# Kernel optimization log

Hardware: AMD Instinct MI355X
Metric: run time of the kernel (lower is better)

## Reference

```python
import jax, jax.numpy as jnp
import numpy as np

EPS = 1e-6
HEADS = 8


def _block_weights(gh, gw):
    # block centers at (i+0.5, j+0.5); 'cos' transform, column-normalized (sum over dim 0)
    ii, jj = np.meshgrid(np.arange(gh) + 0.5, np.arange(gw) + 0.5, indexing='ij')
    centers = np.stack([ii.ravel(), jj.ravel()], axis=-1)  # [N, 2]
    d = np.linalg.norm(centers[:, None, :] - centers[None, :, :], axis=-1)  # [N, N]
    mat = np.cos(d / d.max() * np.pi / 4.0)
    mat = mat / mat.sum(axis=0, keepdims=True)
    return jnp.asarray(mat, dtype=jnp.float32)


def setup_inputs() -> dict:
    key = jax.random.key(0)
    ks = jax.random.split(key, 5)
    B, N, W, C = 8, 256, 49, 512
    s = 1.0 / np.sqrt(C)
    return {
        'x': jax.random.normal(ks[0], (B, N, W, C), jnp.float32),
        'ln_g': jnp.ones((C,), jnp.float32),
        'ln_b': jnp.zeros((C,), jnp.float32),
        'w_qkv': jax.random.normal(ks[1], (3 * C, C), jnp.float32) * s,  # Linear(dim, 3*dim, bias=False)
        'lepe_w': jax.random.normal(ks[2], (C, 1, 5, 5), jnp.float32) * 0.2,  # depthwise 5x5
        'lepe_b': jnp.zeros((C,), jnp.float32),
        'w_out': jax.random.normal(ks[3], (C, C), jnp.float32) * s,
        'b_out': jnp.zeros((C,), jnp.float32),
    }


def reference(x, ln_g, ln_b, w_qkv, lepe_w, lepe_b, w_out, b_out):
    B, N, Wn, C = x.shape
    H = HEADS
    D = C // H
    gh = gw = int(round(N ** 0.5))   # grid of window blocks
    wh = ww = int(round(Wn ** 0.5))  # tokens per window side

    # LayerNorm over channel dim (torch eps=1e-5, biased var)
    mu = x.mean(-1, keepdims=True)
    var = x.var(-1, keepdims=True)
    xn = (x - mu) / jnp.sqrt(var + 1e-5) * ln_g + ln_b

    # qkv projection
    qkv = jnp.einsum('bnwc,oc->bnwo', xn, w_qkv)
    q, k, v = jnp.split(qkv, 3, axis=-1)  # each [B, N, W, C]

    # LePE: fold v to image [B, C, gh*wh, gw*ww], depthwise conv 5x5 pad 2, unfold back
    img = v.reshape(B, gh, gw, wh, ww, C).transpose(0, 5, 1, 3, 2, 4).reshape(B, C, gh * wh, gw * ww)
    lepe = jax.lax.conv_general_dilated(
        img, lepe_w, window_strides=(1, 1), padding=((2, 2), (2, 2)),
        dimension_numbers=('NCHW', 'OIHW', 'NCHW'), feature_group_count=C)
    lepe = lepe + lepe_b[None, :, None, None]
    lepe = lepe.reshape(B, C, gh, wh, gw, ww).transpose(0, 2, 4, 3, 5, 1).reshape(B, N, Wn, C)

    # ReLU + eps feature maps (qk_norm=False -> identity norms)
    q = jax.nn.relu(q) + EPS
    k = jax.nn.relu(k) + EPS

    # split heads: [B, H, N, W, D]
    def split_heads(t):
        return t.reshape(B, N, Wn, H, D).transpose(0, 3, 1, 2, 4)
    q, k, v = split_heads(q), split_heads(k), split_heads(v)

    # per-block k^T v state: [B, H, N, D, D]
    kv = jnp.einsum('bhnwd,bhnwe->bhnde', k, v)
    weight = _block_weights(gh, gw)  # [N, N]
    kv = jnp.einsum('ij,bhjde->bhide', weight, kv)

    k_sum = k.sum(axis=-2)  # [B, H, N, D]
    qk_sum = jnp.einsum('bhnwd,bhnd->bhnw', q, k_sum)[..., None]  # [B, H, N, W, 1]
    normalizer = jnp.einsum('ij,bhjwo->bhiwo', weight, qk_sum) + EPS

    out = jnp.einsum('bhnwd,bhnde->bhnwe', q, kv) / normalizer  # [B, H, N, W, D]
    out = out.transpose(0, 2, 3, 1, 4).reshape(B, N, Wn, C)
    out = out + lepe
    return jnp.einsum('bnwc,oc->bnwo', out, w_out) + b_out
```

## Files before the change

kernel.cpp:

```cpp
#include <hip/hip_runtime.h>
#include <cstdint>

typedef unsigned short u16;
typedef unsigned int   u32;
typedef u16   u16x8 __attribute__((ext_vector_type(8)));
typedef u16   u16x4 __attribute__((ext_vector_type(4)));
typedef float f32x4 __attribute__((ext_vector_type(4)));
typedef __bf16 bf16x8 __attribute__((ext_vector_type(8)));

#define NB    256
#define WTOK  49
#define CH    512
#define HEADS 8
#define DH    64
#define TOK   100352

__device__ __forceinline__ u16 f2bf(float f) {
  u32 u = __float_as_uint(f);
  u = (u + 0x7FFFu + ((u >> 16) & 1u)) >> 16;
  return (u16)u;
}
__device__ __forceinline__ float bf2f(u16 u) { return __uint_as_float(((u32)u) << 16); }

__device__ __forceinline__ void load_lds16(const void* g, void* l) {
  __builtin_amdgcn_global_load_lds(
      reinterpret_cast<__attribute__((address_space(1))) void*>(reinterpret_cast<uintptr_t>(g)),
      reinterpret_cast<__attribute__((address_space(3))) void*>(reinterpret_cast<uintptr_t>(l)),
      16, 0, 0);
}

__global__ void cvt_f32_bf16(const float* __restrict__ in, u16* __restrict__ out, int n8) {
  int i = blockIdx.x * 256 + threadIdx.x;
  if (i < n8) {
    f32x4 a = *(const f32x4*)(in + (long)i * 8);
    f32x4 b = *(const f32x4*)(in + (long)i * 8 + 4);
    u16x8 o;
    o[0]=f2bf(a[0]); o[1]=f2bf(a[1]); o[2]=f2bf(a[2]); o[3]=f2bf(a[3]);
    o[4]=f2bf(b[0]); o[5]=f2bf(b[1]); o[6]=f2bf(b[2]); o[7]=f2bf(b[3]);
    *(u16x8*)(out + (long)i * 8) = o;
  }
}

__global__ void prep_wle(const float* __restrict__ lepe_w, float* __restrict__ wle) {
  int i = blockIdx.x * 256 + threadIdx.x;
  if (i < 12800) {
    int c = i / 25, kk = i % 25;
    wle[kk * 512 + c] = lepe_w[i];
  }
}

__global__ void weight_kernel(u16* __restrict__ Wbf, float* __restrict__ Wt) {
  int j = blockIdx.x, i = threadIdx.x;
  float iy = (float)(i >> 4) + 0.5f, ix = (float)(i & 15) + 0.5f;
  float jy = (float)(j >> 4) + 0.5f, jx = (float)(j & 15) + 0.5f;
  float dy = iy - jy, dx = ix - jx;
  float d = sqrtf(dy * dy + dx * dx);
  const float dmax = 21.213203435596427f;
  float m = cosf(d * (0.78539816339744831f / dmax));
  __shared__ float red[256];
  red[i] = m;
  __syncthreads();
  for (int s = 128; s > 0; s >>= 1) {
    if (i < s) red[i] += red[i + s];
    __syncthreads();
  }
  float w = m / red[0];
  Wbf[i * 256 + j] = f2bf(w);
  Wt[j * 256 + i] = w;
}

__global__ __launch_bounds__(256) void ln_kernel(const float* __restrict__ x,
                                                 const float* __restrict__ g,
                                                 const float* __restrict__ bta,
                                                 u16* __restrict__ xn) {
  int wave = threadIdx.x >> 6, lane = threadIdx.x & 63;
  long t = (long)blockIdx.x * 4 + wave;
  const float* xp = x + t * CH + lane * 8;
  f32x4 a = *(const f32x4*)xp;
  f32x4 b = *(const f32x4*)(xp + 4);
  float s  = a[0]+a[1]+a[2]+a[3]+b[0]+b[1]+b[2]+b[3];
  float sq = a[0]*a[0]+a[1]*a[1]+a[2]*a[2]+a[3]*a[3]+b[0]*b[0]+b[1]*b[1]+b[2]*b[2]+b[3]*b[3];
  for (int m = 1; m < 64; m <<= 1) { s += __shfl_xor(s, m); sq += __shfl_xor(sq, m); }
  float mu = s * (1.0f / 512.0f);
  float var = sq * (1.0f / 512.0f) - mu * mu;
  float rstd = rsqrtf(var + 1e-5f);
  const float* gp = g + lane * 8;
  const float* bp = bta + lane * 8;
  f32x4 g0 = *(const f32x4*)gp, g1 = *(const f32x4*)(gp + 4);
  f32x4 b0 = *(const f32x4*)bp, b1 = *(const f32x4*)(bp + 4);
  u16x8 o;
  o[0] = f2bf((a[0]-mu)*rstd*g0[0] + b0[0]);
  o[1] = f2bf((a[1]-mu)*rstd*g0[1] + b0[1]);
  o[2] = f2bf((a[2]-mu)*rstd*g0[2] + b0[2]);
  o[3] = f2bf((a[3]-mu)*rstd*g0[3] + b0[3]);
  o[4] = f2bf((b[0]-mu)*rstd*g1[0] + b1[0]);
  o[5] = f2bf((b[1]-mu)*rstd*g1[1] + b1[1]);
  o[6] = f2bf((b[2]-mu)*rstd*g1[2] + b1[2]);
  o[7] = f2bf((b[3]-mu)*rstd*g1[3] + b1[3]);
  *(u16x8*)(xn + t * CH + lane * 8) = o;
}

template <int KT>
__device__ __forceinline__ void kstepD(char* sm, const u16* sA, const u16* sB,
                                       int t, int lane_off, int wm, int wn,
                                       f32x4 (&acc)[4][4]) {
  if constexpr (KT + 1 < 16) {
    char* d = sm + ((KT + 1) & 1) * 24576 + t * 16;
    load_lds16(sA + (KT + 1) * 32, d);
    load_lds16(sA + 128 * 512 + (KT + 1) * 32, d + 8192);
    load_lds16(sB + (KT + 1) * 32, d + 16384);
  }
  const char* base = sm + (KT & 1) * 24576 + lane_off;
  bf16x8 fa[4], fb[4];
#pragma unroll
  for (int m = 0; m < 4; m++) fa[m] = *(const bf16x8*)(base + (wm * 4 + m) * 1024);
#pragma unroll
  for (int n = 0; n < 4; n++) fb[n] = *(const bf16x8*)(base + 16384 + (wn * 4 + n) * 1024);
  __builtin_amdgcn_s_setprio(1);
#pragma unroll
  for (int m = 0; m < 4; m++)
#pragma unroll
    for (int n = 0; n < 4; n++)
      acc[m][n] = __builtin_amdgcn_mfma_f32_16x16x32_bf16(fa[m], fb[n], acc[m][n], 0, 0, 0);
  __builtin_amdgcn_s_setprio(0);
  if constexpr (KT + 1 < 16) __syncthreads();
}

template <int EPI>
__global__ __launch_bounds__(512, 4)
void gemmD(const u16* __restrict__ A, const u16* __restrict__ B,
           void* __restrict__ C, u16* __restrict__ vimg,
           const float* __restrict__ bias, int ldc, int nbn) {
  __shared__ __align__(16) char sm[49152];
  const int nwg = gridDim.x, bid = blockIdx.x;
  const int cpx = nwg >> 3;
  const int vid = (bid & 7) * cpx + (bid >> 3);
  const int bn = vid % nbn, bm = vid / nbn;
  const int t = threadIdx.x, lane = t & 63, wave = t >> 6;
  const int wm = wave >> 1, wn = wave & 1;
  const int fr = lane & 15, fq = lane >> 4;
  const int lane_off = (fr >> 1) * 128 + ((((fr & 1) << 2) + fq) ^ (fr >> 1)) * 16;
  const int sl = (t & 7) ^ ((t >> 3) & 7);
  const u16* sA = A + ((long)bm * 256 + ((t >> 3) << 1) + (sl >> 2)) * 512 + (sl & 3) * 8;
  const u16* sB = B + ((long)bn * 128 + ((t >> 3) << 1) + (sl >> 2)) * 512 + (sl & 3) * 8;
  f32x4 acc[4][4] = {};
  {
    char* d = sm + t * 16;
    load_lds16(sA, d);
    load_lds16(sA + 128 * 512, d + 8192);
    load_lds16(sB, d + 16384);
  }
  __syncthreads();
  kstepD<0>(sm, sA, sB, t, lane_off, wm, wn, acc);
  kstepD<1>(sm, sA, sB, t, lane_off, wm, wn, acc);
  kstepD<2>(sm, sA, sB, t, lane_off, wm, wn, acc);
  kstepD<3>(sm, sA, sB, t, lane_off, wm, wn, acc);
  kstepD<4>(sm, sA, sB, t, lane_off, wm, wn, acc);
  kstepD<5>(sm, sA, sB, t, lane_off, wm, wn, acc);
  kstepD<6>(sm, sA, sB, t, lane_off, wm, wn, acc);
  kstepD<7>(sm, sA, sB, t, lane_off, wm, wn, acc);
  kstepD<8>(sm, sA, sB, t, lane_off, wm, wn, acc);
  kstepD<9>(sm, sA, sB, t, lane_off, wm, wn, acc);
  kstepD<10>(sm, sA, sB, t, lane_off, wm, wn, acc);
  kstepD<11>(sm, sA, sB, t, lane_off, wm, wn, acc);
  kstepD<12>(sm, sA, sB, t, lane_off, wm, wn, acc);
  kstepD<13>(sm, sA, sB, t, lane_off, wm, wn, acc);
  kstepD<14>(sm, sA, sB, t, lane_off, wm, wn, acc);
  kstepD<15>(sm, sA, sB, t, lane_off, wm, wn, acc);
  __syncthreads();
  {
    float* ep = (float*)sm + wave * 1088;
    const long r0 = (long)bm * 256 + wm * 64;
    const int c0 = bn * 128 + wn * 64;
    const int rrow = lane >> 2;
    const int cb = (lane & 3) * 16;
    const int cc = c0 + cb;
#pragma unroll
    for (int m = 0; m < 4; m++) {
#pragma unroll
      for (int n = 0; n < 4; n++) {
        int c = c0 + n * 16 + fr;
        float badd = (EPI == 2) ? bias[c] : 0.0f;
#pragma unroll
        for (int jj = 0; jj < 4; jj++) {
          float v = acc[m][n][jj];
          if (EPI == 1) { if (c < 1024) v = fmaxf(v, 0.0f) + 1e-6f; }
          if (EPI == 2) v += badd;
          ep[(fq * 4 + jj) * 68 + n * 16 + fr] = v;
        }
      }
      f32x4 rr[4];
#pragma unroll
      for (int i = 0; i < 4; i++)
        rr[i] = *(const f32x4*)&ep[rrow * 68 + cb + i * 4];
      long gr = r0 + m * 16 + rrow;
      if (EPI == 2) {
        float* gp = (float*)C + gr * ldc + cc;
#pragma unroll
        for (int i = 0; i < 4; i++) *(f32x4*)(gp + i * 4) = rr[i];
      } else {
        u16x8 o0, o1;
#pragma unroll
        for (int i = 0; i < 4; i++) {
          o0[i] = f2bf(rr[0][i]); o0[4 + i] = f2bf(rr[1][i]);
          o1[i] = f2bf(rr[2][i]); o1[4 + i] = f2bf(rr[3][i]);
        }
        u16* gp;
        if (cc < 1024) {
          gp = (u16*)C + gr * ldc + cc;
        } else {
          int tok = (int)gr;
          int b2 = tok / 12544;
          int rem = tok - b2 * 12544;
          int nn = rem / 49;
          int w = rem - nn * 49;
          int wi = w / 7, wj = w - wi * 7;
          int y = (nn >> 4) * 7 + wi + 2;
          int xx = (nn & 15) * 7 + wj + 2;
          gp = vimg + (((long)(b2 * 116 + y)) * 116 + xx) * 512 + (cc - 1024);
        }
        *(u16x8*)gp = o0;
        *(u16x8*)(gp + 8) = o1;
      }
    }
  }
}

template <int EPI>
__global__ __launch_bounds__(256)
void gemm_bt(const u16* __restrict__ A, const u16* __restrict__ B,
             void* __restrict__ C, const float* __restrict__ bias,
             int M, int N, int K, long sAb, long sBb, long sCb) {
  __shared__ u16 As[128 * 32];
  __shared__ u16 Bs[128 * 32];
  const int tid = threadIdx.x;
  const int lane = tid & 63;
  const int wave = tid >> 6;
  const int fr = lane & 15, fq = lane >> 4;
  const int wr = (wave >> 1) * 64, wc = (wave & 1) * 64;
  const long bm = blockIdx.y, bn = blockIdx.x, bz = blockIdx.z;
  const u16* Ab = A + bz * sAb + bm * 128 * (long)K;
  const u16* Bb = B + bz * sBb + bn * 128 * (long)K;
  const int srow = tid >> 2;
  const int scol = (tid & 3) * 8;
  f32x4 acc[4][4] = {};
  for (int k0 = 0; k0 < K; k0 += 32) {
    load_lds16(Ab + (long)srow * K + k0 + scol, As + tid * 8);
    load_lds16(Ab + (long)(srow + 64) * K + k0 + scol, As + 2048 + tid * 8);
    load_lds16(Bb + (long)srow * K + k0 + scol, Bs + tid * 8);
    load_lds16(Bb + (long)(srow + 64) * K + k0 + scol, Bs + 2048 + tid * 8);
    __syncthreads();
    bf16x8 af[4], bf[4];
#pragma unroll
    for (int m = 0; m < 4; m++) af[m] = *(const bf16x8*)&As[(wr + m * 16 + fr) * 32 + fq * 8];
#pragma unroll
    for (int n = 0; n < 4; n++) bf[n] = *(const bf16x8*)&Bs[(wc + n * 16 + fr) * 32 + fq * 8];
#pragma unroll
    for (int m = 0; m < 4; m++)
#pragma unroll
      for (int n = 0; n < 4; n++)
        acc[m][n] = __builtin_amdgcn_mfma_f32_16x16x32_bf16(af[m], bf[n], acc[m][n], 0, 0, 0);
    __syncthreads();
  }
#pragma unroll
  for (int m = 0; m < 4; m++) {
    int r0 = wr + m * 16 + fq * 4;
#pragma unroll
    for (int n = 0; n < 4; n++) {
      int c = (int)bn * 128 + wc + n * 16 + fr;
#pragma unroll
      for (int jj = 0; jj < 4; jj++) {
        long r = bm * 128 + r0 + jj;
        float v = acc[m][n][jj];
        if (EPI == 1) { if (c < 1024) v = fmaxf(v, 0.0f) + 1e-6f; }
        if (EPI == 2) {
          ((float*)C)[bz * sCb + r * N + c] = v + bias[c];
        } else {
          ((u16*)C)[bz * sCb + r * N + c] = f2bf(v);
        }
      }
    }
  }
}

__global__ __launch_bounds__(256)
void zero_border(u16* __restrict__ vimg) {
  int y = blockIdx.x, b = blockIdx.y;
  int tid = threadIdx.x;
  u16* row = vimg + ((long)(b * 116 + y)) * 116 * 512;
  u16x8 z = {};
  if (y < 2 || y >= 114) {
    for (int i = tid; i < 116 * 512 / 8; i += 256) *(u16x8*)(row + i * 8) = z;
  } else {
    int col = tid >> 6;
    int x = (col < 2) ? col : 112 + col;
    *(u16x8*)(row + x * 512 + (tid & 63) * 8) = z;
  }
}

__global__ __launch_bounds__(256, 2)
void lepe_conv4(const u16* __restrict__ vimg, const float* __restrict__ wle,
                const float* __restrict__ lb, u16* __restrict__ lepe) {
  const int tid = threadIdx.x;
  const int c0 = (tid & 127) * 4;
  const int x0 = blockIdx.x * 4 + (tid >> 7) * 2;
  const int ys = blockIdx.y * 14;
  const int b  = blockIdx.z;
  f32x4 wv[25];
#pragma unroll
  for (int k = 0; k < 25; k++) wv[k] = *(const f32x4*)(wle + k * 512 + c0);
  const f32x4 bias = *(const f32x4*)(lb + c0);
  const u16* rbase = vimg + (((long)(b * 116 + ys)) * 116 + x0) * 512 + c0;
  u16x4 win[5][6];
#pragma unroll
  for (int j = 0; j < 4; j++) {
    const u16* rp = rbase + (long)j * (116 * 512);
#pragma unroll
    for (int kx = 0; kx < 6; kx++) win[j][kx] = *(const u16x4*)(rp + kx * 512);
  }
  const int gj0 = x0 / 7, wj0 = x0 - gj0 * 7;
  const int gj1 = (x0 + 1) / 7, wj1 = (x0 + 1) - gj1 * 7;
  u16* ob0 = lepe + (((long)(b * 256 + blockIdx.y * 32 + gj0)) * 49 + wj0) * 512 + c0;
  u16* ob1 = lepe + (((long)(b * 256 + blockIdx.y * 32 + gj1)) * 49 + wj1) * 512 + c0;
#pragma unroll
  for (int i = 0; i < 14; i++) {
    {
      const u16* rp = rbase + (long)(i + 4) * (116 * 512);
#pragma unroll
      for (int kx = 0; kx < 6; kx++) win[(i + 4) % 5][kx] = *(const u16x4*)(rp + kx * 512);
    }
    f32x4 a0 = bias, a1 = bias;
#pragma unroll
    for (int s = 0; s < 5; s++)
#pragma unroll
      for (int kx = 0; kx < 5; kx++) {
        u16x4 v0 = win[(i + s) % 5][kx];
        u16x4 v1 = win[(i + s) % 5][kx + 1];
        f32x4 w = wv[s * 5 + kx];
#pragma unroll
        for (int c = 0; c < 4; c++) {
          a0[c] += bf2f(v0[c]) * w[c];
          a1[c] += bf2f(v1[c]) * w[c];
        }
      }
    u16x4 o0, o1;
#pragma unroll
    for (int c = 0; c < 4; c++) { o0[c] = f2bf(a0[c]); o1[c] = f2bf(a1[c]); }
    long so = (long)((i / 7) * 784 + (i % 7) * 7) * 512;
    *(u16x4*)(ob0 + so) = o0;
    *(u16x4*)(ob1 + so) = o1;
  }
}

__global__ __launch_bounds__(256)
void kv_local_kernel(const u16* __restrict__ qk, const u16* __restrict__ vimg,
                     u16* __restrict__ KVl, float* __restrict__ qk_sum) {
  int n = blockIdx.x, h = blockIdx.y, b = blockIdx.z;
  int bh = b * HEADS + h;
  long tbase = ((long)(b * NB + n)) * WTOK;
  const int gi = n >> 4, gj = n & 15;
  __shared__ u16 kT[64 * 72];
  __shared__ u16 vT[64 * 72];
  __shared__ u16 qs[49 * 72];
  __shared__ float ksum[64];
  __shared__ float qkp[256];
  int tid = threadIdx.x;
  for (int i = tid; i < (64 * 72) / 2; i += 256) {
    ((u32*)kT)[i] = 0;
    ((u32*)vT)[i] = 0;
  }
  __syncthreads();
  {
    int w = tid >> 3, d0 = (tid & 7) * 8;
    u16x8 k8 = *(const u16x8*)(qk + (tbase + w) * 1024 + 512 + h * 64 + d0);
    int wi = w / 7, wj = w - wi * 7;
    long va = (((long)(b * 116 + gi * 7 + wi + 2)) * 116 + (gj * 7 + wj + 2)) * 512 + h * 64 + d0;
    u16x8 v8 = *(const u16x8*)(vimg + va);
#pragma unroll
    for (int i = 0; i < 8; i++) { kT[(d0 + i) * 72 + w] = k8[i]; vT[(d0 + i) * 72 + w] = v8[i]; }
    int w2 = w + 32;
    if (w2 < WTOK) {
      u16x8 k82 = *(const u16x8*)(qk + (tbase + w2) * 1024 + 512 + h * 64 + d0);
      int wi2 = w2 / 7, wj2 = w2 - wi2 * 7;
      long va2 = (((long)(b * 116 + gi * 7 + wi2 + 2)) * 116 + (gj * 7 + wj2 + 2)) * 512 + h * 64 + d0;
      u16x8 v82 = *(const u16x8*)(vimg + va2);
#pragma unroll
      for (int i = 0; i < 8; i++) { kT[(d0 + i) * 72 + w2] = k82[i]; vT[(d0 + i) * 72 + w2] = v82[i]; }
    }
    if (tid < 196) {
      int wq = tid >> 2, dq = (tid & 3) * 16;
      u16x8 q0 = *(const u16x8*)(qk + (tbase + wq) * 1024 + h * 64 + dq);
      u16x8 q1 = *(const u16x8*)(qk + (tbase + wq) * 1024 + h * 64 + dq + 8);
      *(u16x8*)&qs[wq * 72 + dq] = q0;
      *(u16x8*)&qs[wq * 72 + dq + 8] = q1;
    }
  }
  __syncthreads();
  if (tid < 64) {
    float s = 0.0f;
#pragma unroll
    for (int c = 0; c < 9; c++) {
      u16x8 r = *(const u16x8*)&kT[tid * 72 + c * 8];
#pragma unroll
      for (int i = 0; i < 8; i++) s += bf2f(r[i]);
    }
    ksum[tid] = s;
  }
  __syncthreads();
  if (tid < 196) {
    int w = tid >> 2, d0 = (tid & 3) * 16;
    float s = 0.0f;
#pragma unroll
    for (int i = 0; i < 16; i++) s += bf2f(qs[w * 72 + d0 + i]) * ksum[d0 + i];
    qkp[tid] = s;
  }
  __syncthreads();
  if (tid < WTOK) {
    float s = qkp[tid * 4] + qkp[tid * 4 + 1] + qkp[tid * 4 + 2] + qkp[tid * 4 + 3];
    qk_sum[((long)bh * NB + n) * WTOK + tid] = s;
  }
  int lane = tid & 63, wave = tid >> 6;
  int fr = lane & 15, fq = lane >> 4;
  f32x4 acc[4] = {};
#pragma unroll
  for (int ks = 0; ks < 2; ks++) {
    bf16x8 a = *(const bf16x8*)&kT[(wave * 16 + fr) * 72 + ks * 32 + fq * 8];
#pragma unroll
    for (int n4 = 0; n4 < 4; n4++) {
      bf16x8 bb = *(const bf16x8*)&vT[(n4 * 16 + fr) * 72 + ks * 32 + fq * 8];
      acc[n4] = __builtin_amdgcn_mfma_f32_16x16x32_bf16(a, bb, acc[n4], 0, 0, 0);
    }
  }
  long obase = ((long)bh * NB + n) * 4096;
#pragma unroll
  for (int n4 = 0; n4 < 4; n4++)
#pragma unroll
    for (int jj = 0; jj < 4; jj++) {
      int d = wave * 16 + fq * 4 + jj;
      int e = n4 * 16 + fr;
      KVl[obase + d * 64 + e] = f2bf(acc[n4][jj]);
    }
}

__global__ __launch_bounds__(256)
void transpose_kv(const u16* __restrict__ in, u16* __restrict__ out) {
  int dt = blockIdx.x, jt = blockIdx.y, bh = blockIdx.z;
  __shared__ u16 t[64 * 72];
  int tid = threadIdx.x;
  {
    int jr = tid >> 2, c0 = (tid & 3) * 16;
    const u16* ip = in + ((long)bh * NB + jt * 64 + jr) * 4096 + dt * 64 + c0;
    *(u16x8*)&t[jr * 72 + c0] = *(const u16x8*)ip;
    *(u16x8*)&t[jr * 72 + c0 + 8] = *(const u16x8*)(ip + 8);
  }
  __syncthreads();
  {
    int der = tid >> 2, j0 = (tid & 3) * 16;
    u16x8 o0, o1;
#pragma unroll
    for (int i = 0; i < 8; i++) o0[i] = t[(j0 + i) * 72 + der];
#pragma unroll
    for (int i = 0; i < 8; i++) o1[i] = t[(j0 + 8 + i) * 72 + der];
    u16* op = out + ((long)bh * 4096 + dt * 64 + der) * 256 + jt * 64 + j0;
    *(u16x8*)op = o0;
    *(u16x8*)(op + 8) = o1;
  }
}

__global__ __launch_bounds__(256)
void norm_kernel(const float* __restrict__ Wt, const float* __restrict__ qk_sum,
                 float* __restrict__ inv_norm) {
  int bh = blockIdx.x, tid = threadIdx.x;
  __shared__ float qk[NB * WTOK];
  for (int i = tid; i < NB * WTOK; i += 256) qk[i] = qk_sum[(long)bh * NB * WTOK + i];
  __syncthreads();
  float acc[WTOK];
#pragma unroll
  for (int w = 0; w < WTOK; w++) acc[w] = 0.0f;
  for (int j = 0; j < NB; j++) {
    float wv = Wt[j * NB + tid];
#pragma unroll
    for (int w = 0; w < WTOK; w++) acc[w] += wv * qk[j * WTOK + w];
  }
  long ob = ((long)bh * NB + tid) * WTOK;
#pragma unroll
  for (int w = 0; w < WTOK; w++) inv_norm[ob + w] = 1.0f / (acc[w] + 1e-6f);
}

__global__ __launch_bounds__(256)
void attn_out_kernel(const u16* __restrict__ qk, const u16* __restrict__ kvm,
                     const float* __restrict__ inv_norm, const u16* __restrict__ lepe,
                     u16* __restrict__ ebuf) {
  int n = blockIdx.x, h = blockIdx.y, b = blockIdx.z;
  int bh = b * HEADS + h;
  long tbase = ((long)(b * NB + n)) * WTOK;
  __shared__ u16 qs[64 * 72];
  __shared__ u16 kvT[64 * 72];
  __shared__ float inv[WTOK];
  int tid = threadIdx.x;
  if (tid < 196) {
    int w = tid >> 2, d0 = (tid & 3) * 16;
    u16x8 q0 = *(const u16x8*)(qk + (tbase + w) * 1024 + h * 64 + d0);
    u16x8 q1 = *(const u16x8*)(qk + (tbase + w) * 1024 + h * 64 + d0 + 8);
    *(u16x8*)&qs[w * 72 + d0] = q0;
    *(u16x8*)&qs[w * 72 + d0 + 8] = q1;
  }
  {
    int d = tid >> 2, e0 = (tid & 3) * 16;
    const u16* kp = kvm + ((long)bh * NB + n) * 4096 + d * 64 + e0;
    u16x8 k0 = *(const u16x8*)kp;
    u16x8 k1 = *(const u16x8*)(kp + 8);
#pragma unroll
    for (int i = 0; i < 8; i++) { kvT[(e0 + i) * 72 + d] = k0[i]; kvT[(e0 + 8 + i) * 72 + d] = k1[i]; }
  }
  if (tid < WTOK) inv[tid] = inv_norm[((long)bh * NB + n) * WTOK + tid];
  __syncthreads();
  int lane = tid & 63, wave = tid >> 6;
  int fr = lane & 15, fq = lane >> 4;
  f32x4 acc[4] = {};
#pragma unroll
  for (int ks = 0; ks < 2; ks++) {
    bf16x8 a = *(const bf16x8*)&qs[(wave * 16 + fr) * 72 + ks * 32 + fq * 8];
#pragma unroll
    for (int n4 = 0; n4 < 4; n4++) {
      bf16x8 bb = *(const bf16x8*)&kvT[(n4 * 16 + fr) * 72 + ks * 32 + fq * 8];
      acc[n4] = __builtin_amdgcn_mfma_f32_16x16x32_bf16(a, bb, acc[n4], 0, 0, 0);
    }
  }
#pragma unroll
  for (int n4 = 0; n4 < 4; n4++)
#pragma unroll
    for (int jj = 0; jj < 4; jj++) {
      int w = wave * 16 + fq * 4 + jj;
      if (w < WTOK) {
        int e = n4 * 16 + fr;
        long off = (tbase + w) * CH + h * 64 + e;
        float v = acc[n4][jj] * inv[w] + bf2f(lepe[off]);
        ebuf[off] = f2bf(v);
      }
    }
}

static const size_t OFF_XN    = 0;
static const size_t OFF_QKV   = 102760448;
static const size_t OFF_EBUF  = OFF_QKV + 205520896;
static const size_t OFF_KVL   = OFF_QKV + 308281344;
static const size_t OFF_KVT   = OFF_KVL + 134217728;
static const size_t OFF_QKS   = OFF_KVT + 134217728;
static const size_t OFF_INV   = OFF_QKS + 3211264;
static const size_t OFF_WBF   = OFF_INV + 3211264;
static const size_t OFF_WTF   = OFF_WBF + 131072;
static const size_t OFF_WQKVB = OFF_WTF + 262144;
static const size_t OFF_WOUTB = OFF_WQKVB + 1572864;
static const size_t OFF_WLE   = OFF_WOUTB + 524288;

extern "C" void kernel_launch(void* const* d_in, const int* in_sizes, int n_in,
                              void* d_out, int out_size, void* d_ws, size_t ws_size,
                              hipStream_t stream) {
  const float* x      = (const float*)d_in[0];
  const float* ln_g   = (const float*)d_in[1];
  const float* ln_b   = (const float*)d_in[2];
  const float* w_qkv  = (const float*)d_in[3];
  const float* lepe_w = (const float*)d_in[4];
  const float* lepe_b = (const float*)d_in[5];
  const float* w_out  = (const float*)d_in[6];
  const float* b_out  = (const float*)d_in[7];
  float* out = (float*)d_out;
  char* ws = (char*)d_ws;

  u16*   xn     = (u16*)(ws + OFF_XN);
  u16*   lepe   = (u16*)(ws + OFF_XN);
  u16*   qk     = (u16*)(ws + OFF_QKV);
  u16*   ebuf   = (u16*)(ws + OFF_EBUF);
  u16*   KVl    = (u16*)(ws + OFF_KVL);
  u16*   kvm    = (u16*)(ws + OFF_KVL);
  u16*   vimg   = (u16*)(ws + OFF_KVT);
  u16*   KVT    = (u16*)(ws + OFF_KVT);
  float* qks    = (float*)(ws + OFF_QKS);
  float* invn   = (float*)(ws + OFF_INV);
  u16*   Wbf    = (u16*)(ws + OFF_WBF);
  float* Wt     = (float*)(ws + OFF_WTF);
  u16*   wqkvb  = (u16*)(ws + OFF_WQKVB);
  u16*   woutb  = (u16*)(ws + OFF_WOUTB);
  float* wle    = (float*)(ws + OFF_WLE);

  cvt_f32_bf16<<<384, 256, 0, stream>>>(w_qkv, wqkvb, 98304);
  cvt_f32_bf16<<<128, 256, 0, stream>>>(w_out, woutb, 32768);
  prep_wle<<<50, 256, 0, stream>>>(lepe_w, wle);
  weight_kernel<<<256, 256, 0, stream>>>(Wbf, Wt);
  zero_border<<<dim3(116, 8), 256, 0, stream>>>(vimg);

  ln_kernel<<<25088, 256, 0, stream>>>(x, ln_g, ln_b, xn);

  gemmD<1><<<4704, 512, 0, stream>>>(xn, wqkvb, (void*)qk, vimg, nullptr, 1024, 12);

  lepe_conv4<<<dim3(28, 8, 8), 256, 0, stream>>>(vimg, wle, lepe_b, lepe);

  kv_local_kernel<<<dim3(NB, HEADS, 8), 256, 0, stream>>>(qk, vimg, KVl, qks);

  transpose_kv<<<dim3(64, 4, 64), 256, 0, stream>>>(KVl, KVT);

  gemm_bt<0><<<dim3(32, 2, 64), 256, 0, stream>>>(Wbf, KVT, (void*)kvm, nullptr,
                                                  NB, 4096, NB,
                                                  0, (long)4096 * 256, (long)256 * 4096);

  norm_kernel<<<64, 256, 0, stream>>>(Wt, qks, invn);

  attn_out_kernel<<<dim3(NB, HEADS, 8), 256, 0, stream>>>(qk, kvm, invn, lepe, ebuf);

  gemmD<2><<<1568, 512, 0, stream>>>(ebuf, woutb, (void*)out, nullptr, b_out, 512, 4);
}
```

Measured before the change: 891.4 us.

## Use 256x256 GEMM tiles with K=64 steps and finer-grained LDS pipelining

```diff
diff --git a/kernel.cpp b/kernel.cpp
--- a/kernel.cpp
+++ b/kernel.cpp
@@ -100,83 +100,156 @@
   *(u16x8*)(xn + t * CH + lane * 8) = o;
 }
 
+#define MFMA_BF16 __builtin_amdgcn_mfma_f32_16x16x32_bf16
+
 template <int KT>
-__device__ __forceinline__ void kstepD(char* sm, const u16* sA, const u16* sB,
-                                       int t, int lane_off, int wm, int wn,
-                                       f32x4 (&acc)[4][4]) {
-  if constexpr (KT + 1 < 16) {
-    char* d = sm + ((KT + 1) & 1) * 24576 + t * 16;
-    load_lds16(sA + (KT + 1) * 32, d);
-    load_lds16(sA + 128 * 512 + (KT + 1) * 32, d + 8192);
-    load_lds16(sB + (KT + 1) * 32, d + 16384);
-  }
-  const char* base = sm + (KT & 1) * 24576 + lane_off;
+__device__ __forceinline__ void ktileT(char* sm, const u16* sAst, const u16* sBst,
+                                       int t, int aoff, int boff,
+                                       f32x4 (&acc)[8][4]) {
+  const char* rb = sm + (KT & 1) * 65536;
+  char* wb = sm + ((KT + 1) & 1) * 65536;
   bf16x8 fa[4], fb[4];
 #pragma unroll
-  for (int m = 0; m < 4; m++) fa[m] = *(const bf16x8*)(base + (wm * 4 + m) * 1024);
-#pragma unroll
-  for (int n = 0; n < 4; n++) fb[n] = *(const bf16x8*)(base + 16384 + (wn * 4 + n) * 1024);
+  for (int m = 0; m < 4; m++) fa[m] = *(const bf16x8*)(rb + aoff + m * 1024);
+#pragma unroll
+  for (int n = 0; n < 4; n++) fb[n] = *(const bf16x8*)(rb + boff + n * 1024);
+  if constexpr (KT + 1 < 8) {
+    const u16* s = sAst + (KT + 1) * 64;
+    char* d = wb + t * 16;
+    load_lds16(s, d);
+    load_lds16(s + 65536, d + 8192);
+  }
+  __builtin_amdgcn_s_barrier();
+  asm volatile("s_waitcnt lgkmcnt(0)" ::: "memory");
+  __builtin_amdgcn_sched_barrier(0);
   __builtin_amdgcn_s_setprio(1);
 #pragma unroll
   for (int m = 0; m < 4; m++)
 #pragma unroll
     for (int n = 0; n < 4; n++)
-      acc[m][n] = __builtin_amdgcn_mfma_f32_16x16x32_bf16(fa[m], fb[n], acc[m][n], 0, 0, 0);
+      acc[m][n] = MFMA_BF16(fa[m], fb[n], acc[m][n], 0, 0, 0);
   __builtin_amdgcn_s_setprio(0);
-  if constexpr (KT + 1 < 16) __syncthreads();
+  __builtin_amdgcn_s_barrier();
+#pragma unroll
+  for (int m = 0; m < 4; m++) fa[m] = *(const bf16x8*)(rb + aoff + (4 + m) * 1024);
+  if constexpr (KT + 1 < 8) {
+    const u16* s = sBst + (KT + 1) * 64;
+    char* d = wb + 32768 + t * 16;
+    load_lds16(s, d);
+    load_lds16(s + 65536, d + 8192);
+  }
+  __builtin_amdgcn_s_barrier();
+  asm volatile("s_waitcnt lgkmcnt(0)" ::: "memory");
+  __builtin_amdgcn_sched_barrier(0);
+  __builtin_amdgcn_s_setprio(1);
+#pragma unroll
+  for (int m = 0; m < 4; m++)
+#pragma unroll
+    for (int n = 0; n < 4; n++)
+      acc[4 + m][n] = MFMA_BF16(fa[m], fb[n], acc[4 + m][n], 0, 0, 0);
+  __builtin_amdgcn_s_setprio(0);
+  if constexpr (KT < 7) {
+    asm volatile("s_waitcnt vmcnt(4)" ::: "memory");
+  } else {
+    asm volatile("s_waitcnt vmcnt(0)" ::: "memory");
+  }
+  __builtin_amdgcn_s_barrier();
+#pragma unroll
+  for (int m = 0; m < 4; m++) fa[m] = *(const bf16x8*)(rb + 16384 + aoff + m * 1024);
+#pragma unroll
+  for (int n = 0; n < 4; n++) fb[n] = *(const bf16x8*)(rb + 16384 + boff + n * 1024);
+  if constexpr (KT + 1 < 8) {
+    const u16* s = sAst + (KT + 1) * 64 + 32;
+    char* d = wb + 16384 + t * 16;
+    load_lds16(s, d);
+    load_lds16(s + 65536, d + 8192);
+  }
+  __builtin_amdgcn_s_barrier();
+  asm volatile("s_waitcnt lgkmcnt(0)" ::: "memory");
+  __builtin_amdgcn_sched_barrier(0);
+  __builtin_amdgcn_s_setprio(1);
+#pragma unroll
+  for (int m = 0; m < 4; m++)
+#pragma unroll
+    for (int n = 0; n < 4; n++)
+      acc[m][n] = MFMA_BF16(fa[m], fb[n], acc[m][n], 0, 0, 0);
+  __builtin_amdgcn_s_setprio(0);
+  __builtin_amdgcn_s_barrier();
+#pragma unroll
+  for (int m = 0; m < 4; m++) fa[m] = *(const bf16x8*)(rb + 16384 + aoff + (4 + m) * 1024);
+  if constexpr (KT + 1 < 8) {
+    const u16* s = sBst + (KT + 1) * 64 + 32;
+    char* d = wb + 49152 + t * 16;
+    load_lds16(s, d);
+    load_lds16(s + 65536, d + 8192);
+  }
+  __builtin_amdgcn_s_barrier();
+  asm volatile("s_waitcnt lgkmcnt(0)" ::: "memory");
+  __builtin_amdgcn_sched_barrier(0);
+  __builtin_amdgcn_s_setprio(1);
+#pragma unroll
+  for (int m = 0; m < 4; m++)
+#pragma unroll
+    for (int n = 0; n < 4; n++)
+      acc[4 + m][n] = MFMA_BF16(fa[m], fb[n], acc[4 + m][n], 0, 0, 0);
+  __builtin_amdgcn_s_setprio(0);
+  if constexpr (KT < 7) {
+    asm volatile("s_waitcnt vmcnt(4)" ::: "memory");
+  }
+  __builtin_amdgcn_s_barrier();
 }
 
 template <int EPI>
-__global__ __launch_bounds__(512, 4)
-void gemmD(const u16* __restrict__ A, const u16* __restrict__ B,
+__global__ __launch_bounds__(512, 2)
+void gemmT(const u16* __restrict__ A, const u16* __restrict__ B,
            void* __restrict__ C, u16* __restrict__ vimg,
            const float* __restrict__ bias, int ldc, int nbn) {
-  __shared__ __align__(16) char sm[49152];
+  __shared__ __align__(16) char sm[131072];
   const int nwg = gridDim.x, bid = blockIdx.x;
   const int cpx = nwg >> 3;
   const int vid = (bid & 7) * cpx + (bid >> 3);
   const int bn = vid % nbn, bm = vid / nbn;
   const int t = threadIdx.x, lane = t & 63, wave = t >> 6;
-  const int wm = wave >> 1, wn = wave & 1;
+  const int wm = wave >> 2, wn = wave & 3;
   const int fr = lane & 15, fq = lane >> 4;
-  const int lane_off = (fr >> 1) * 128 + ((((fr & 1) << 2) + fq) ^ (fr >> 1)) * 16;
-  const int sl = (t & 7) ^ ((t >> 3) & 7);
-  const u16* sA = A + ((long)bm * 256 + ((t >> 3) << 1) + (sl >> 2)) * 512 + (sl & 3) * 8;
-  const u16* sB = B + ((long)bn * 128 + ((t >> 3) << 1) + (sl >> 2)) * 512 + (sl & 3) * 8;
-  f32x4 acc[4][4] = {};
+  const int kcolsw = ((t & 3) * 8) ^ (((t >> 5) & 1) * 16);
+  const u16* sAst = A + ((long)bm * 256 + (t >> 2)) * 512 + kcolsw;
+  const u16* sBst = B + ((long)bn * 256 + (t >> 2)) * 512 + kcolsw;
+  const int fsw = (fq * 16) ^ ((fr >> 3) << 5);
+  const int aoff = (wm * 128 + fr) * 64 + fsw;
+  const int boff = 32768 + (wn * 64 + fr) * 64 + fsw;
+  f32x4 acc[8][4] = {};
   {
-    char* d = sm + t * 16;
-    load_lds16(sA, d);
-    load_lds16(sA + 128 * 512, d + 8192);
-    load_lds16(sB, d + 16384);
-  }
-  __syncthreads();
-  kstepD<0>(sm, sA, sB, t, lane_off, wm, wn, acc);
-  kstepD<1>(sm, sA, sB, t, lane_off, wm, wn, acc);
-  kstepD<2>(sm, sA, sB, t, lane_off, wm, wn, acc);
-  kstepD<3>(sm, sA, sB, t, lane_off, wm, wn, acc);
-  kstepD<4>(sm, sA, sB, t, lane_off, wm, wn, acc);
-  kstepD<5>(sm, sA, sB, t, lane_off, wm, wn, acc);
-  kstepD<6>(sm, sA, sB, t, lane_off, wm, wn, acc);
-  kstepD<7>(sm, sA, sB, t, lane_off, wm, wn, acc);
-  kstepD<8>(sm, sA, sB, t, lane_off, wm, wn, acc);
-  kstepD<9>(sm, sA, sB, t, lane_off, wm, wn, acc);
-  kstepD<10>(sm, sA, sB, t, lane_off, wm, wn, acc);
-  kstepD<11>(sm, sA, sB, t, lane_off, wm, wn, acc);
-  kstepD<12>(sm, sA, sB, t, lane_off, wm, wn, acc);
-  kstepD<13>(sm, sA, sB, t, lane_off, wm, wn, acc);
-  kstepD<14>(sm, sA, sB, t, lane_off, wm, wn, acc);
-  kstepD<15>(sm, sA, sB, t, lane_off, wm, wn, acc);
-  __syncthreads();
+    char* d0 = sm + t * 16;
+    load_lds16(sAst, d0);
+    load_lds16(sAst + 65536, d0 + 8192);
+    load_lds16(sBst, d0 + 32768);
+    load_lds16(sBst + 65536, d0 + 40960);
+    __builtin_amdgcn_sched_barrier(0);
+    load_lds16(sAst + 32, d0 + 16384);
+    load_lds16(sAst + 65536 + 32, d0 + 24576);
+    load_lds16(sBst + 32, d0 + 49152);
+    load_lds16(sBst + 65536 + 32, d0 + 57344);
+  }
+  asm volatile("s_waitcnt vmcnt(4)" ::: "memory");
+  __builtin_amdgcn_s_barrier();
+  ktileT<0>(sm, sAst, sBst, t, aoff, boff, acc);
+  ktileT<1>(sm, sAst, sBst, t, aoff, boff, acc);
+  ktileT<2>(sm, sAst, sBst, t, aoff, boff, acc);
+  ktileT<3>(sm, sAst, sBst, t, aoff, boff, acc);
+  ktileT<4>(sm, sAst, sBst, t, aoff, boff, acc);
+  ktileT<5>(sm, sAst, sBst, t, aoff, boff, acc);
+  ktileT<6>(sm, sAst, sBst, t, aoff, boff, acc);
+  ktileT<7>(sm, sAst, sBst, t, aoff, boff, acc);
   {
     float* ep = (float*)sm + wave * 1088;
-    const long r0 = (long)bm * 256 + wm * 64;
-    const int c0 = bn * 128 + wn * 64;
+    const long r0 = (long)bm * 256 + wm * 128;
+    const int c0 = bn * 256 + wn * 64;
     const int rrow = lane >> 2;
     const int cb = (lane & 3) * 16;
     const int cc = c0 + cb;
 #pragma unroll
-    for (int m = 0; m < 4; m++) {
+    for (int m = 0; m < 8; m++) {
 #pragma unroll
       for (int n = 0; n < 4; n++) {
         int c = c0 + n * 16 + fr;
@@ -259,7 +332,7 @@
     for (int m = 0; m < 4; m++)
 #pragma unroll
       for (int n = 0; n < 4; n++)
-        acc[m][n] = __builtin_amdgcn_mfma_f32_16x16x32_bf16(af[m], bf[n], acc[m][n], 0, 0, 0);
+        acc[m][n] = MFMA_BF16(af[m], bf[n], acc[m][n], 0, 0, 0);
     __syncthreads();
   }
 #pragma unroll
@@ -428,7 +501,7 @@
 #pragma unroll
     for (int n4 = 0; n4 < 4; n4++) {
       bf16x8 bb = *(const bf16x8*)&vT[(n4 * 16 + fr) * 72 + ks * 32 + fq * 8];
-      acc[n4] = __builtin_amdgcn_mfma_f32_16x16x32_bf16(a, bb, acc[n4], 0, 0, 0);
+      acc[n4] = MFMA_BF16(a, bb, acc[n4], 0, 0, 0);
     }
   }
   long obase = ((long)bh * NB + n) * 4096;
@@ -524,7 +597,7 @@
 #pragma unroll
     for (int n4 = 0; n4 < 4; n4++) {
       bf16x8 bb = *(const bf16x8*)&kvT[(n4 * 16 + fr) * 72 + ks * 32 + fq * 8];
-      acc[n4] = __builtin_amdgcn_mfma_f32_16x16x32_bf16(a, bb, acc[n4], 0, 0, 0);
+      acc[n4] = MFMA_BF16(a, bb, acc[n4], 0, 0, 0);
     }
   }
 #pragma unroll
@@ -592,7 +665,7 @@
 
   ln_kernel<<<25088, 256, 0, stream>>>(x, ln_g, ln_b, xn);
 
-  gemmD<1><<<4704, 512, 0, stream>>>(xn, wqkvb, (void*)qk, vimg, nullptr, 1024, 12);
+  gemmT<1><<<2352, 512, 0, stream>>>(xn, wqkvb, (void*)qk, vimg, nullptr, 1024, 6);
 
   lepe_conv4<<<dim3(28, 8, 8), 256, 0, stream>>>(vimg, wle, lepe_b, lepe);
 
@@ -608,5 +681,5 @@
 
   attn_out_kernel<<<dim3(NB, HEADS, 8), 256, 0, stream>>>(qk, kvm, invn, lepe, ebuf);
 
-  gemmD<2><<<1568, 512, 0, stream>>>(ebuf, woutb, (void*)out, nullptr, b_out, 512, 4);
-}
+  gemmT<2><<<784, 512, 0, stream>>>(ebuf, woutb, (void*)out, nullptr, b_out, 512, 2);
+}
```

After: 913.1 us. 2.4% more time.
